# Performance work log

Hardware: AMD Instinct MI355X
Metric: run time of the kernel (lower is better)

The kernel has to match this reference:

```python
import jax, jax.numpy as jnp
import numpy as np

MAX_DISP = 192


def setup_inputs() -> dict:
    key = jax.random.key(0)
    k1, k2 = jax.random.split(key)
    B, C, H, W = 4, 32, 64, 128
    left_feats = jax.random.normal(k1, (B, C, H, W), dtype=jnp.float32)
    right_feats = jax.random.normal(k2, (B, C, H, W), dtype=jnp.float32)
    return {"left_feats": left_feats, "right_feats": right_feats}


def build_cost(left_feats, right_feats, max_disp=MAX_DISP):
    B, C, H, W = left_feats.shape
    D = max_disp // 4
    d = jnp.arange(D)[:, None]          # [D,1]
    w = jnp.arange(W)[None, :]          # [1,W]
    mask = (w >= d).astype(left_feats.dtype)  # [D,W]
    # left half: cost[:, :C, d, :, w] = left[:, :, :, w] for w >= d, else 0
    left_part = left_feats[:, :, None, :, :] * mask[None, None, :, None, :]  # [B,C,D,H,W]
    # right half: cost[:, C:, d, :, w] = right[:, :, :, w-d] for w >= d, else 0
    idx = jnp.clip(w - d, 0, W - 1)     # [D,W]
    right_gather = right_feats[:, :, :, idx]            # [B,C,H,D,W]
    right_part = jnp.transpose(right_gather, (0, 1, 3, 2, 4)) * mask[None, None, :, None, :]
    return jnp.concatenate([left_part, right_part], axis=1)  # [B,2C,D,H,W]


def reference(left_feats, right_feats):
    return build_cost(left_feats, right_feats)
```

## Files before the change

kernel.cpp:

```cpp
#include <hip/hip_runtime.h>


#define BB 4
#define CC 32
#define HH 64
#define WW 128
#define DD 48

typedef float vfloat4 __attribute__((ext_vector_type(4)));

__global__ __launch_bounds__(256) void cost_kernel(
    const float* __restrict__ left,
    const float* __restrict__ right,
    float* __restrict__ out)
{
    const int p  = blockIdx.x * 256 + threadIdx.x;
    const int d  = blockIdx.y;
    const int bc = blockIdx.z;
    const int b  = bc >> 6;
    const int c2 = bc & 63;
    const int h  = p >> 5;
    const int w0 = (p & 31) * 4;

    const bool is_right = (c2 >= CC);
    const int  c        = is_right ? (c2 - CC) : c2;
    const float* __restrict__ src = is_right ? right : left;
    const float* __restrict__ row = src + ((((size_t)b * CC + c) * HH + h) * WW);

    float v[4];
    if (!is_right) {
        const vfloat4 lv = *reinterpret_cast<const vfloat4*>(row + w0);
        v[0] = lv.x; v[1] = lv.y; v[2] = lv.z; v[3] = lv.w;
        if (w0 < d) {
            #pragma unroll
            for (int i = 0; i < 4; ++i)
                if (w0 + i < d) v[i] = 0.0f;
        }
    } else {
        if (d <= w0) {
            #pragma unroll
            for (int i = 0; i < 4; ++i) v[i] = row[w0 + i - d];
        } else if (d > w0 + 3) {
            #pragma unroll
            for (int i = 0; i < 4; ++i) v[i] = 0.0f;
        } else {
            #pragma unroll
            for (int i = 0; i < 4; ++i) {
                const int ws = w0 + i - d;
                v[i] = (ws >= 0) ? row[ws] : 0.0f;
            }
        }
    }

    vfloat4 o;
    o.x = v[0]; o.y = v[1]; o.z = v[2]; o.w = v[3];
    vfloat4* __restrict__ out4 = reinterpret_cast<vfloat4*>(out);
    __builtin_nontemporal_store(o, &out4[((size_t)bc * DD + d) * (HH * WW / 4) + p]);
}

extern "C" void kernel_launch(void* const* d_in, const int* in_sizes, int n_in,
                              void* d_out, int out_size, void* d_ws, size_t ws_size,
                              hipStream_t stream)
{
    const float* left  = (const float*)d_in[0];
    const float* right = (const float*)d_in[1];
    float* out = (float*)d_out;

    dim3 grid(HH * WW / 4 / 256, DD, BB * 2 * CC);
    cost_kernel<<<grid, dim3(256), 0, stream>>>(left, right, out);
}
```

Measured before the change: 422.7 us.

## Loop over all disparities per thread, reusing loaded vectors for shifted outputs

Each thread now produces all 48 disparity slices for its four-pixel group instead of one, with the grid's disparity dimension collapsed to one. Left features are loaded once and masked per disparity. Right features are walked backward one aligned vector at a time, and the four shifted outputs are built by register shuffles. This removes redundant and unaligned global loads and per-block index math, at the cost of fewer, longer-running threads issuing many strided nontemporal stores.

```diff
diff --git a/kernel.cpp b/kernel.cpp
--- a/kernel.cpp
+++ b/kernel.cpp
@@ -15,47 +15,56 @@
     float* __restrict__ out)
 {
     const int p  = blockIdx.x * 256 + threadIdx.x;
-    const int d  = blockIdx.y;
     const int bc = blockIdx.z;
     const int b  = bc >> 6;
     const int c2 = bc & 63;
     const int h  = p >> 5;
-    const int w0 = (p & 31) * 4;
+    const int k0 = p & 31;
+    const int w0 = k0 * 4;
 
     const bool is_right = (c2 >= CC);
     const int  c        = is_right ? (c2 - CC) : c2;
     const float* __restrict__ src = is_right ? right : left;
-    const float* __restrict__ row = src + ((((size_t)b * CC + c) * HH + h) * WW);
+    const vfloat4* __restrict__ row4 =
+        reinterpret_cast<const vfloat4*>(src + ((((size_t)b * CC + c) * HH + h) * WW));
 
-    float v[4];
+    const int stride4 = HH * WW / 4;
+    vfloat4* __restrict__ out4 = reinterpret_cast<vfloat4*>(out)
+                               + (size_t)bc * DD * stride4 + p;
+
     if (!is_right) {
-        const vfloat4 lv = *reinterpret_cast<const vfloat4*>(row + w0);
-        v[0] = lv.x; v[1] = lv.y; v[2] = lv.z; v[3] = lv.w;
-        if (w0 < d) {
-            #pragma unroll
-            for (int i = 0; i < 4; ++i)
-                if (w0 + i < d) v[i] = 0.0f;
+        const vfloat4 lv = row4[k0];
+        #pragma unroll
+        for (int d = 0; d < DD; ++d) {
+            vfloat4 o;
+            o.x = (w0 + 0 >= d) ? lv.x : 0.0f;
+            o.y = (w0 + 1 >= d) ? lv.y : 0.0f;
+            o.z = (w0 + 2 >= d) ? lv.z : 0.0f;
+            o.w = (w0 + 3 >= d) ? lv.w : 0.0f;
+            __builtin_nontemporal_store(o, out4 + (size_t)d * stride4);
         }
     } else {
-        if (d <= w0) {
-            #pragma unroll
-            for (int i = 0; i < 4; ++i) v[i] = row[w0 + i - d];
-        } else if (d > w0 + 3) {
-            #pragma unroll
-            for (int i = 0; i < 4; ++i) v[i] = 0.0f;
-        } else {
-            #pragma unroll
-            for (int i = 0; i < 4; ++i) {
-                const int ws = w0 + i - d;
-                v[i] = (ws >= 0) ? row[ws] : 0.0f;
-            }
+        vfloat4 b4 = row4[k0];
+        int k = k0;
+        #pragma unroll
+        for (int g = 0; g < DD / 4; ++g) {
+            vfloat4 a4 = (vfloat4)(0.0f);
+            if (k >= 1) a4 = row4[k - 1];
+
+            const vfloat4 o0 = b4;
+            vfloat4 o1; o1.x = a4.w; o1.y = b4.x; o1.z = b4.y; o1.w = b4.z;
+            vfloat4 o2; o2.x = a4.z; o2.y = a4.w; o2.z = b4.x; o2.w = b4.y;
+            vfloat4 o3; o3.x = a4.y; o3.y = a4.z; o3.z = a4.w; o3.w = b4.x;
+
+            __builtin_nontemporal_store(o0, out4 + (size_t)(4 * g + 0) * stride4);
+            __builtin_nontemporal_store(o1, out4 + (size_t)(4 * g + 1) * stride4);
+            __builtin_nontemporal_store(o2, out4 + (size_t)(4 * g + 2) * stride4);
+            __builtin_nontemporal_store(o3, out4 + (size_t)(4 * g + 3) * stride4);
+
+            b4 = a4;
+            --k;
         }
     }
-
-    vfloat4 o;
-    o.x = v[0]; o.y = v[1]; o.z = v[2]; o.w = v[3];
-    vfloat4* __restrict__ out4 = reinterpret_cast<vfloat4*>(out);
-    __builtin_nontemporal_store(o, &out4[((size_t)bc * DD + d) * (HH * WW / 4) + p]);
 }
 
 extern "C" void kernel_launch(void* const* d_in, const int* in_sizes, int n_in,
@@ -66,6 +75,6 @@
     const float* right = (const float*)d_in[1];
     float* out = (float*)d_out;
 
-    dim3 grid(HH * WW / 4 / 256, DD, BB * 2 * CC);
+    dim3 grid(HH * WW / 4 / 256, 1, BB * 2 * CC);
     cost_kernel<<<grid, dim3(256), 0, stream>>>(left, right, out);
 }
```

New measurement: 391.6 us. 1.08x faster.

## Loop over disparities per block, reusing register-held input slabs

Applied to the files above, without the earlier changes.

Each block now handles a full (b,c) slab across half of the disparity range. Input rows stay in registers and are reused over 24 disparities. For the right half, shifted vectors are built by register permutation of the two adjacent float4 loads rather than unaligned scalar loads. The grid shrinks to 512 blocks, each writing many float4s. The nontemporal store builtin is dropped in favour of plain stores, which may change cache behaviour on this write-bound output. Fewer blocks may also limit memory-level parallelism.

```diff
diff --git a/kernel.cpp b/kernel.cpp
--- a/kernel.cpp
+++ b/kernel.cpp
@@ -6,6 +6,8 @@
 #define HH 64
 #define WW 128
 #define DD 48
+#define DHALF 24
+#define SLAB4 2048
 
 typedef float vfloat4 __attribute__((ext_vector_type(4)));
 
@@ -14,48 +16,91 @@
     const float* __restrict__ right,
     float* __restrict__ out)
 {
-    const int p  = blockIdx.x * 256 + threadIdx.x;
-    const int d  = blockIdx.y;
-    const int bc = blockIdx.z;
-    const int b  = bc >> 6;
-    const int c2 = bc & 63;
-    const int h  = p >> 5;
-    const int w0 = (p & 31) * 4;
+    const int id    = blockIdx.x;
+    const int bc    = id >> 1;
+    const int dhalf = id & 1;
+    const int d0    = dhalf * DHALF;
 
+    const int t  = threadIdx.x;
+    const int k0 = t & 31;
+    const int hb = t >> 5;
+    const int w0 = k0 * 4;
+
+    const int  b        = bc >> 6;
+    const int  c2       = bc & 63;
     const bool is_right = (c2 >= CC);
     const int  c        = is_right ? (c2 - CC) : c2;
     const float* __restrict__ src = is_right ? right : left;
-    const float* __restrict__ row = src + ((((size_t)b * CC + c) * HH + h) * WW);
+    const vfloat4* __restrict__ src4 =
+        reinterpret_cast<const vfloat4*>(src + (size_t)(b * CC + c) * HH * WW);
 
-    float v[4];
+    vfloat4* __restrict__ op = reinterpret_cast<vfloat4*>(out)
+                             + ((size_t)bc * DD + d0) * SLAB4 + t;
+
+    const vfloat4 zero = (vfloat4)(0.0f);
+
     if (!is_right) {
-        const vfloat4 lv = *reinterpret_cast<const vfloat4*>(row + w0);
-        v[0] = lv.x; v[1] = lv.y; v[2] = lv.z; v[3] = lv.w;
-        if (w0 < d) {
+        vfloat4 Lv[8];
+        #pragma unroll
+        for (int i = 0; i < 8; ++i)
+            Lv[i] = src4[(hb + 8 * i) * 32 + k0];
+
+        #pragma unroll 1
+        for (int dd = 0; dd < DHALF; ++dd, op += SLAB4) {
+            const int d = d0 + dd;
             #pragma unroll
-            for (int i = 0; i < 4; ++i)
-                if (w0 + i < d) v[i] = 0.0f;
+            for (int i = 0; i < 8; ++i) {
+                vfloat4 o;
+                o.x = (w0 + 0 >= d) ? Lv[i].x : 0.0f;
+                o.y = (w0 + 1 >= d) ? Lv[i].y : 0.0f;
+                o.z = (w0 + 2 >= d) ? Lv[i].z : 0.0f;
+                o.w = (w0 + 3 >= d) ? Lv[i].w : 0.0f;
+                op[i * 256] = o;
+            }
         }
     } else {
-        if (d <= w0) {
+        const int q0 = d0 >> 2;
+        vfloat4 Av[8], Bv[8];
+        #pragma unroll
+        for (int i = 0; i < 8; ++i) {
+            const int base = (hb + 8 * i) * 32;
+            int kB = k0 - q0, kA = k0 - q0 - 1;
+            vfloat4 vB = src4[base + (kB >= 0 ? kB : 0)];
+            vfloat4 vA = src4[base + (kA >= 0 ? kA : 0)];
+            Bv[i] = (kB >= 0) ? vB : zero;
+            Av[i] = (kA >= 0) ? vA : zero;
+        }
+
+        #pragma unroll 1
+        for (int qg = 0; qg < DHALF / 4; ++qg, op += 4 * SLAB4) {
+            const int q = q0 + qg;
+
+            vfloat4 Tv[8];
             #pragma unroll
-            for (int i = 0; i < 4; ++i) v[i] = row[w0 + i - d];
-        } else if (d > w0 + 3) {
+            for (int i = 0; i < 8; ++i) {
+                const int kk = k0 - q - 2;
+                vfloat4 v = src4[(hb + 8 * i) * 32 + (kk >= 0 ? kk : 0)];
+                Tv[i] = (kk >= 0) ? v : zero;
+            }
+
             #pragma unroll
-            for (int i = 0; i < 4; ++i) v[i] = 0.0f;
-        } else {
+            for (int s = 0; s < 4; ++s) {
+                #pragma unroll
+                for (int i = 0; i < 8; ++i) {
+                    const vfloat4 B = Bv[i], A = Av[i];
+                    vfloat4 o;
+                    if      (s == 0) { o = B; }
+                    else if (s == 1) { o.x = A.w; o.y = B.x; o.z = B.y; o.w = B.z; }
+                    else if (s == 2) { o.x = A.z; o.y = A.w; o.z = B.x; o.w = B.y; }
+                    else             { o.x = A.y; o.y = A.z; o.z = A.w; o.w = B.x; }
+                    op[s * SLAB4 + i * 256] = o;
+                }
+            }
+
             #pragma unroll
-            for (int i = 0; i < 4; ++i) {
-                const int ws = w0 + i - d;
-                v[i] = (ws >= 0) ? row[ws] : 0.0f;
-            }
+            for (int i = 0; i < 8; ++i) { Bv[i] = Av[i]; Av[i] = Tv[i]; }
         }
     }
-
-    vfloat4 o;
-    o.x = v[0]; o.y = v[1]; o.z = v[2]; o.w = v[3];
-    vfloat4* __restrict__ out4 = reinterpret_cast<vfloat4*>(out);
-    __builtin_nontemporal_store(o, &out4[((size_t)bc * DD + d) * (HH * WW / 4) + p]);
 }
 
 extern "C" void kernel_launch(void* const* d_in, const int* in_sizes, int n_in,
@@ -66,6 +111,5 @@
     const float* right = (const float*)d_in[1];
     float* out = (float*)d_out;
 
-    dim3 grid(HH * WW / 4 / 256, DD, BB * 2 * CC);
-    cost_kernel<<<grid, dim3(256), 0, stream>>>(left, right, out);
+    cost_kernel<<<dim3(512), dim3(256), 0, stream>>>(left, right, out);
 }
```

Result: faster. 398.4 us (-5.7%).
